# Optimization experiments

Measured on AMD Instinct MI355X. Metric: run time of the kernel, lower is better.

## Reference

```python
import jax, jax.numpy as jnp
import numpy as np

B, T, I = 256, 1024, 64
P, E, NOUT = 256, 128, 64
K = 2
TEMP = 8.0
LN_EPS = 1e-5


def setup_inputs() -> dict:
    key = jax.random.key(0)
    ks = jax.random.split(key, 10)
    lim_in = 1.0 / np.sqrt(I)
    lim_e = 1.0 / np.sqrt(E)
    return {
        "x": jax.random.normal(ks[0], (B, T, I), dtype=jnp.float32),
        "pointer_init": jax.random.uniform(ks[1], (B,), dtype=jnp.float32) * P,
        "W_in": jax.random.uniform(ks[2], (E, I), minval=-lim_in, maxval=lim_in),
        "b_in": jax.random.uniform(ks[3], (E,), minval=-lim_in, maxval=lim_in),
        "ln_w": jnp.ones((E,), jnp.float32),
        "ln_b": jnp.zeros((E,), jnp.float32),
        "jump_dest": jax.random.uniform(ks[4], (P,), dtype=jnp.float32) * P,
        "Wg": jax.random.uniform(ks[5], (1, E), minval=-lim_e, maxval=lim_e),
        "bg": jax.random.uniform(ks[6], (1,), minval=-lim_e, maxval=lim_e),
        "context_strength": jnp.float32(0.2),
        "Wo": jax.random.uniform(ks[7], (NOUT, E), minval=-lim_e, maxval=lim_e),
        "bo": jax.random.uniform(ks[8], (NOUT,), minval=-lim_e, maxval=lim_e),
    }


def _layer_norm(h, w, b):
    mu = jnp.mean(h, axis=-1, keepdims=True)
    var = jnp.mean((h - mu) ** 2, axis=-1, keepdims=True)
    return (h - mu) * jax.lax.rsqrt(var + LN_EPS) * w + b


def reference(x, pointer_init, W_in, b_in, ln_w, ln_b, jump_dest, Wg, bg, context_strength, Wo, bo):
    Bsz = x.shape[0]
    nP = jump_dest.shape[0]
    offsets = jnp.arange(-K, K + 1, dtype=jnp.int32)  # [5]
    batch_idx = jnp.arange(Bsz)[:, None]               # [B,1]
    ctx_scale = jax.nn.sigmoid(context_strength)
    half = nP / 2.0

    def step(carry, x_t):
        mem, hid, ptr = carry                          # [B,P,E], [B,E], [B]
        emb = jnp.tanh(x_t @ W_in.T + b_in)            # [B,E]
        base = jnp.clip(jnp.floor(ptr).astype(jnp.int32), 0, nP - 1)
        idx = jnp.mod(base[:, None] + offsets[None, :], nP)  # [B,5]
        delta = jnp.mod(idx.astype(x_t.dtype) - ptr[:, None] + half, nP) - half
        w = jax.nn.softmax(-(delta ** 2) / TEMP, axis=1)     # [B,5]
        nbh = jnp.take_along_axis(mem, idx[:, :, None], axis=1)  # [B,5,E]
        ctx = jnp.sum(w[:, :, None] * nbh, axis=1)               # [B,E]
        su = jnp.tanh(emb + ctx_scale * ctx + hid)               # [B,E]
        hid_new = _layer_norm(su, ln_w, ln_b)
        mem_new = mem.at[batch_idx, idx].add(w[:, :, None] * su[:, None, :])
        cur = jnp.clip(ptr.astype(jnp.int32), 0, nP - 1)
        jt = jump_dest[cur]                                      # [B]
        jl = (su @ Wg.T + bg)[:, 0]                              # [B]
        probs = jax.nn.sigmoid(jl)
        sj = (probs > 0.5).astype(x_t.dtype) - jax.lax.stop_gradient(probs) + probs
        walk = jnp.mod(ptr + 1.0, nP)
        ptr_new = jnp.where(sj > 0.5, jt, walk)
        return (mem_new, hid_new, ptr_new), None

    mem0 = jnp.zeros((Bsz, nP, W_in.shape[0]), x.dtype)
    hid0 = jnp.zeros((Bsz, W_in.shape[0]), x.dtype)
    (mem, hid, ptr), _ = jax.lax.scan(step, (mem0, hid0, pointer_init), jnp.swapaxes(x, 0, 1))
    logits = hid @ Wo.T + bo
    return logits
```

## Files before the change

### kernel.cpp

```cpp
#include <hip/hip_runtime.h>
#include <math.h>

#define Bn    256
#define Tn    1024
#define In    64
#define Pn    256
#define En    128
#define NOUTn 64
#define LN_EPS 1e-5f

#define C1f 0.3606737602222409f
#define K1f 0.8824969025845955f
#define K2f 0.6065306597126334f

typedef float f32x2 __attribute__((ext_vector_type(2)));

__device__ __forceinline__ float tanh_fast(float x) {
    float e = __builtin_amdgcn_exp2f(x * 2.88539008177793f);
    return 1.0f - 2.0f * __builtin_amdgcn_rcpf(e + 1.0f);
}
__device__ __forceinline__ f32x2 tanh2(f32x2 x) {
    f32x2 e;
    e[0] = __builtin_amdgcn_exp2f(x[0] * 2.88539008177793f);
    e[1] = __builtin_amdgcn_exp2f(x[1] * 2.88539008177793f);
    f32x2 r;
    r[0] = __builtin_amdgcn_rcpf(e[0] + 1.0f);
    r[1] = __builtin_amdgcn_rcpf(e[1] + 1.0f);
    return 1.0f - 2.0f * r;
}

template<int CTRL, int RMASK>
__device__ __forceinline__ float dpp_add(float x) {
    return x + __int_as_float(__builtin_amdgcn_update_dpp(
        0, __float_as_int(x), CTRL, RMASK, 0xF, false));
}
__device__ __forceinline__ void wave_sum64_x3(float& x, float& y, float& z) {
#define LVL(C, R) x = dpp_add<C, R>(x); y = dpp_add<C, R>(y); z = dpp_add<C, R>(z);
    LVL(0x111, 0xF)
    LVL(0x112, 0xF)
    LVL(0x114, 0xF)
    LVL(0x118, 0xF)
    LVL(0x142, 0xA)
    LVL(0x143, 0xC)
#undef LVL
    x = __int_as_float(__builtin_amdgcn_readlane(__float_as_int(x), 63));
    y = __int_as_float(__builtin_amdgcn_readlane(__float_as_int(y), 63));
    z = __int_as_float(__builtin_amdgcn_readlane(__float_as_int(z), 63));
}

#define STAGE_FLOATS (3 * 16 * En)
#define LDSF_FLOATS  (Pn * En + Pn + STAGE_FLOATS)
#define LDSF_BYTES   (LDSF_FLOATS * 4)

__global__ __launch_bounds__(192, 1)
void fused2_kernel(const float* __restrict__ x,
                   const float* __restrict__ pointer_init,
                   const float* __restrict__ W_in, const float* __restrict__ b_in,
                   const float* __restrict__ ln_w, const float* __restrict__ ln_b,
                   const float* __restrict__ jump_dest,
                   const float* __restrict__ Wg,  const float* __restrict__ bg,
                   const float* __restrict__ cs_ptr,
                   const float* __restrict__ Wo,  const float* __restrict__ bo,
                   float* __restrict__ out) {
    extern __shared__ float lds[];
    float* mem = lds;
    float* jd  = lds + Pn * En;
    float* stg = lds + Pn * En + Pn;

    const int b   = blockIdx.x;
    const int tid = threadIdx.x;

    if (tid >= 64) {
        const int p    = tid - 64;
        const int tq   = p >> 5;
        const int eidx = p & 31;
        float be[4];
        #pragma unroll
        for (int j = 0; j < 4; ++j) be[j] = b_in[eidx + 32 * j];
        const float* xb = x + (size_t)b * Tn * In;

#define PRODUCE(K, BUF) {                                                     \
    const int t0 = (K) * 16 + tq * 4;                                         \
    const float4* xr = (const float4*)(xb + t0 * In);      \
    float acc[4][4];                                                          \
    _Pragma("unroll")                                                         \
    for (int tt = 0; tt < 4; ++tt)                                            \
        _Pragma("unroll")                                                     \
        for (int j = 0; j < 4; ++j) acc[tt][j] = 0.f;                         \
    _Pragma("unroll")                                                         \
    for (int i4 = 0; i4 < 16; ++i4) {                                         \
        float4 xv[4];                                                         \
        _Pragma("unroll")                                                     \
        for (int tt = 0; tt < 4; ++tt) xv[tt] = xr[tt * 16 + i4];             \
        float4 wf[4];                                                         \
        _Pragma("unroll")                                                     \
        for (int j = 0; j < 4; ++j)                                           \
            wf[j] = *(const float4*)(W_in + (eidx + 32 * j) * In + i4 * 4);   \
        _Pragma("unroll")                                                     \
        for (int tt = 0; tt < 4; ++tt)                                        \
            _Pragma("unroll")                                                 \
            for (int j = 0; j < 4; ++j) {                                     \
                acc[tt][j] += xv[tt].x * wf[j].x;                             \
                acc[tt][j] += xv[tt].y * wf[j].y;                             \
                acc[tt][j] += xv[tt].z * wf[j].z;                             \
                acc[tt][j] += xv[tt].w * wf[j].w;                             \
            }                                                                 \
    }                                                                         \
    float* sg = stg + (BUF) * 2048 + tq * 512;                                \
    _Pragma("unroll")                                                         \
    for (int j = 0; j < 4; ++j) {                                             \
        float4 o;                                                             \
        o.x = tanh_fast(acc[0][j] + be[j]);                                   \
        o.y = tanh_fast(acc[1][j] + be[j]);                                   \
        o.z = tanh_fast(acc[2][j] + be[j]);                                   \
        o.w = tanh_fast(acc[3][j] + be[j]);                                   \
        *(float4*)(sg + (eidx + 32 * j) * 4) = o;                             \
    }                                                                         \
}
        PRODUCE(0, 0)
        PRODUCE(1, 1)
        __syncthreads();
        int buf = 2;
        for (int k = 0; k < 64; ++k) {
            if (k + 2 < 64) {
                PRODUCE(k + 2, buf)
                buf = (buf == 2) ? 0 : buf + 1;
            }
            __syncthreads();
        }
#undef PRODUCE
        __syncthreads();
        return;
    }

    const int l = tid;

    float4* m4 = (float4*)mem;
    for (int i = l; i < Pn * En / 4; i += 64) m4[i] = make_float4(0.f, 0.f, 0.f, 0.f);
    for (int i = l; i < Pn; i += 64) jd[i] = jump_dest[i];

    const f32x2 lnw = {ln_w[l], ln_w[l + 64]};
    const f32x2 lnb = {ln_b[l], ln_b[l + 64]};
    const f32x2 wg  = {Wg[l],   Wg[l + 64]};
    const float bgs = bg[0];
    const float cs  = 1.0f / (1.0f + expf(-cs_ptr[0]));
    f32x2 hid = {0.f, 0.f};

    float* myb = mem + 2 * l;

    float jl = 1.0f;
    float z0 = 0.f, z1 = 0.f, z2 = 1.f, z3 = 0.f, z4 = 0.f, inv = 1.f;
    float ptrW = 0.f; int baseW = 0; float jtW_pre = 0.f;
    f32x2 wnb0 = {0,0}, wnb1 = {0,0}, wnb2 = {0,0}, wnb3 = {0,0}, wnb4 = {0,0};
    float *wp0 = myb, *wp1 = myb, *wp2 = myb, *wp3 = myb, *wp4 = myb;
    float jptr  = pointer_init[b];
    int   jbase = (int)jptr; jbase = jbase > 255 ? 255 : jbase;
    float jz0, jz1, jz2 = 1.f, jz3, jz4, jinv;
    {
        const float frac = jptr - (float)jbase;
        const float r  = __builtin_amdgcn_exp2f(frac * C1f);
        const float ri = __builtin_amdgcn_exp2f(-frac * C1f);
        jz0 = K2f * ri * ri; jz1 = K1f * ri;
        jz3 = K1f * r;       jz4 = K2f * r * r;
        jinv = __builtin_amdgcn_rcpf(((jz0 + jz1) + (jz2 + jz3)) + jz4);
    }
    float *jp0 = mem + (((jbase + 254) & 255) << 7) + 2 * l;
    float *jp1 = mem + (((jbase + 255) & 255) << 7) + 2 * l;
    float *jp2 = mem + ((jbase) << 7) + 2 * l;
    float *jp3 = mem + (((jbase + 1) & 255) << 7) + 2 * l;
    float *jp4 = mem + (((jbase + 2) & 255) << 7) + 2 * l;
    f32x2 jnb0, jnb1, jnb2, jnb3, jnb4;
    float jjt;

    __syncthreads();

    jnb0 = *(f32x2*)jp0; jnb1 = *(f32x2*)jp1; jnb2 = *(f32x2*)jp2;
    jnb3 = *(f32x2*)jp3; jnb4 = *(f32x2*)jp4;
    jjt  = jd[jbase];

    const float* sa0 = stg + 4 * l;
    float4 A0 = *(const float4*)sa0;
    float4 A1 = *(const float4*)(sa0 + 256);

#define SSTEP(EC0, EC1) {                                                      \
    const bool JMP = jl > 0.0f;                         \
                  \
    const f32x2 ctxW = inv  * (((wnb0 * z0  + wnb1 * z1 )                      \
                              + (wnb2 * z2  + wnb3 * z3 )) + wnb4 * z4 );      \
    const f32x2 ctxJ = jinv * (((jnb0 * jz0 + jnb1 * jz1)                      \
                              + (jnb2 * jz2 + jnb3 * jz3)) + jnb4 * jz4);      \
    f32x2 ctx; ctx[0] = JMP ? ctxJ[0] : ctxW[0];                               \
               ctx[1] = JMP ? ctxJ[1] : ctxW[1];                               \
               \
    const float ptr  = JMP ? jptr  : ptrW;                                     \
    const int   base = JMP ? jbase : baseW;                                    \
    z0 = JMP ? jz0 : z0;  z1 = JMP ? jz1 : z1;                                 \
    z3 = JMP ? jz3 : z3;  z4 = JMP ? jz4 : z4;                                 \
    inv = JMP ? jinv : inv;                                                    \
    const f32x2 nb0 = JMP ? jnb0 : wnb0;                                       \
    const f32x2 nb1 = JMP ? jnb1 : wnb1;                                       \
    const f32x2 nb2 = JMP ? jnb2 : wnb2;                                       \
    const f32x2 nb3 = JMP ? jnb3 : wnb3;                                       \
    const f32x2 nb4 = JMP ? jnb4 : wnb4;                                       \
    float* p0 = JMP ? jp0 : wp0;  float* p1 = JMP ? jp1 : wp1;                 \
    float* p2 = JMP ? jp2 : wp2;  float* p3 = JMP ? jp3 : wp3;                 \
    float* p4 = JMP ? jp4 : wp4;                                               \
    const float jt_n = JMP ? jjt : jtW_pre;                                    \
                                      \
    f32x2 em; em[0] = (EC0); em[1] = (EC1);                                    \
    const f32x2 su = tanh2(em + cs * ctx + hid);                               \
    const f32x2 g  = su * inv;                                                 \
    const f32x2 m0v = nb0 + z0 * g, m1v = nb1 + z1 * g, m2v = nb2 + z2 * g,    \
                m3v = nb3 + z3 * g, m4v = nb4 + z4 * g;                        \
    *(f32x2*)p0 = m0v; *(f32x2*)p1 = m1v; *(f32x2*)p2 = m2v;                   \
    *(f32x2*)p3 = m3v; *(f32x2*)p4 = m4v;                                      \
      \
    baseW = (base + 1) & 255;                                                  \
    ptrW  = ptr + 1.0f; if (ptrW >= 256.0f) ptrW -= 256.0f;                    \
    wnb0 = m1v; wnb1 = m2v; wnb2 = m3v; wnb3 = m4v;                            \
    wp0 = p1; wp1 = p2; wp2 = p3; wp3 = p4;                                    \
    wp4 = mem + (((base + 3) & 255) << 7) + 2 * l;                             \
    wnb4 = *(f32x2*)wp4;                                                       \
    jtW_pre = jd[baseW];                                                       \
                 \
    jptr  = jt_n;                                                              \
    jbase = (int)jptr; jbase = jbase > 255 ? 255 : jbase;                      \
    {                                                                          \
        const float frac = jptr - (float)jbase;                                \
        const float r  = __builtin_amdgcn_exp2f(frac * C1f);                   \
        const float ri = __builtin_amdgcn_exp2f(-frac * C1f);                  \
        jz0 = K2f * ri * ri; jz1 = K1f * ri;                                   \
        jz3 = K1f * r;       jz4 = K2f * r * r;                                \
        jinv = __builtin_amdgcn_rcpf(((jz0 + jz1) + (jz2 + jz3)) + jz4);       \
    }                                                                          \
    jp0 = mem + (((jbase + 254) & 255) << 7) + 2 * l;                          \
    jp1 = mem + (((jbase + 255) & 255) << 7) + 2 * l;                          \
    jp2 = mem + ((jbase) << 7) + 2 * l;                                        \
    jp3 = mem + (((jbase + 1) & 255) << 7) + 2 * l;                            \
    jp4 = mem + (((jbase + 2) & 255) << 7) + 2 * l;                            \
    jnb0 = *(f32x2*)jp0; jnb1 = *(f32x2*)jp1; jnb2 = *(f32x2*)jp2;             \
    jnb3 = *(f32x2*)jp3; jnb4 = *(f32x2*)jp4;                                  \
    jjt  = jd[jbase];                                                          \
                                       \
    float s1 = su[0] + su[1];                                                  \
    const f32x2 sq = su * su;  float s2 = sq[0] + sq[1];                       \
    const f32x2 sg = su * wg;  float s3 = sg[0] + sg[1];                       \
    wave_sum64_x3(s1, s2, s3);                                                 \
    const float mu   = s1 * (1.0f / En);                                       \
    const float var  = s2 * (1.0f / En) - mu * mu;                             \
    const float rstd = __builtin_amdgcn_rsqf(var + LN_EPS);                    \
    hid = (su - mu) * rstd * lnw + lnb;                                        \
    jl  = s3 + bgs;                                                            \
}

    for (int k = 0; k < 64; ++k) {
        #pragma unroll 1
        for (int gi = 0; gi < 4; ++gi) {
            const int tb  = k * 4 + gi;
            int tbn = tb + 1; if (tbn > 255) tbn = 255;
            const float* sb = stg + ((tbn >> 2) % 3) * 2048 + (tbn & 3) * 512 + 4 * l;
            float4 B0 = *(const float4*)sb;
            float4 B1 = *(const float4*)(sb + 256);
            SSTEP(A0.x, A1.x)
            SSTEP(A0.y, A1.y)
            SSTEP(A0.z, A1.z)
            SSTEP(A0.w, A1.w)
            A0 = B0; A1 = B1;
        }
        __syncthreads();
    }
#undef SSTEP

    mem[l] = hid[0]; mem[64 + l] = hid[1];
    __syncthreads();
    const float4* w4 = (const float4*)(Wo + l * En);
    const float4* h4 = (const float4*)mem;
    float a0 = 0.f, a1 = 0.f, a2 = 0.f, a3 = 0.f;
    #pragma unroll
    for (int i = 0; i < En / 4; ++i) {
        float4 wv = w4[i]; float4 hv = h4[i];
        a0 += wv.x * hv.x; a1 += wv.y * hv.y; a2 += wv.z * hv.z; a3 += wv.w * hv.w;
    }
    out[b * NOUTn + l] = (a0 + a1) + (a2 + a3) + bo[l];
}

extern "C" void kernel_launch(void* const* d_in, const int* in_sizes, int n_in,
                              void* d_out, int out_size, void* d_ws, size_t ws_size,
                              hipStream_t stream) {
    const float* x            = (const float*)d_in[0];
    const float* pointer_init = (const float*)d_in[1];
    const float* W_in         = (const float*)d_in[2];
    const float* b_in         = (const float*)d_in[3];
    const float* ln_w         = (const float*)d_in[4];
    const float* ln_b         = (const float*)d_in[5];
    const float* jump_dest    = (const float*)d_in[6];
    const float* Wg           = (const float*)d_in[7];
    const float* bg           = (const float*)d_in[8];
    const float* cs           = (const float*)d_in[9];
    const float* Wo           = (const float*)d_in[10];
    const float* bo           = (const float*)d_in[11];
    float* out = (float*)d_out;
    (void)d_ws; (void)ws_size;

    (void)hipFuncSetAttribute((const void*)fused2_kernel,
                              hipFuncAttributeMaxDynamicSharedMemorySize, LDSF_BYTES);
    fused2_kernel<<<Bn, 192, LDSF_BYTES, stream>>>(
        x, pointer_init, W_in, b_in, ln_w, ln_b, jump_dest, Wg, bg, cs,
        Wo, bo, out);
}
```

Before: 483.0 us.

## Split embedding GEMM into separate kernel and stream scan inputs from global

Replaces the fused producer/consumer kernel, whose two extra wavefronts computed the input embedding into a triple-buffered LDS stage, with two kernels. A parallel emb_kernel writes the tanh embeddings to workspace, and a single-wave scan_kernel reads them from global memory with one-group-ahead prefetch. This drops the per-chunk __syncthreads and the producer work that shared the CU with the serial scan. In exchange it adds a global round trip of B*T*E floats through the workspace, and a global load latency on the scan's critical path.

```diff
diff --git a/kernel.cpp b/kernel.cpp
--- a/kernel.cpp
+++ b/kernel.cpp
@@ -48,92 +48,81 @@
     z = __int_as_float(__builtin_amdgcn_readlane(__float_as_int(z), 63));
 }
 
-#define STAGE_FLOATS (3 * 16 * En)
-#define LDSF_FLOATS  (Pn * En + Pn + STAGE_FLOATS)
-#define LDSF_BYTES   (LDSF_FLOATS * 4)
-
-__global__ __launch_bounds__(192, 1)
-void fused2_kernel(const float* __restrict__ x,
-                   const float* __restrict__ pointer_init,
-                   const float* __restrict__ W_in, const float* __restrict__ b_in,
-                   const float* __restrict__ ln_w, const float* __restrict__ ln_b,
-                   const float* __restrict__ jump_dest,
-                   const float* __restrict__ Wg,  const float* __restrict__ bg,
-                   const float* __restrict__ cs_ptr,
-                   const float* __restrict__ Wo,  const float* __restrict__ bo,
-                   float* __restrict__ out) {
+
+__global__ __launch_bounds__(256, 2)
+void emb_kernel(const float* __restrict__ x,
+                const float* __restrict__ W_in, const float* __restrict__ b_in,
+                float* __restrict__ emb) {
+    const int b    = blockIdx.x >> 4;
+    const int tc   = blockIdx.x & 15;
+    const int tid  = threadIdx.x;
+    const int tq   = tid >> 4;
+    const int eidx = tid & 15;
+
+    const int t0 = tc * 64 + tq * 4;
+    const float4* xr = (const float4*)(x + ((size_t)b * Tn + t0) * In);
+
+    float be[8];
+    #pragma unroll
+    for (int j = 0; j < 8; ++j) be[j] = b_in[eidx + 16 * j];
+
+    float acc[4][8];
+    #pragma unroll
+    for (int tt = 0; tt < 4; ++tt)
+        #pragma unroll
+        for (int j = 0; j < 8; ++j) acc[tt][j] = 0.f;
+
+    #pragma unroll
+    for (int i4 = 0; i4 < 16; ++i4) {
+        float4 xv[4];
+        #pragma unroll
+        for (int tt = 0; tt < 4; ++tt) xv[tt] = xr[tt * 16 + i4];
+        float4 wf[8];
+        #pragma unroll
+        for (int j = 0; j < 8; ++j)
+            wf[j] = *(const float4*)(W_in + (eidx + 16 * j) * In + i4 * 4);
+        #pragma unroll
+        for (int tt = 0; tt < 4; ++tt)
+            #pragma unroll
+            for (int j = 0; j < 8; ++j) {
+                acc[tt][j] += xv[tt].x * wf[j].x;
+                acc[tt][j] += xv[tt].y * wf[j].y;
+                acc[tt][j] += xv[tt].z * wf[j].z;
+                acc[tt][j] += xv[tt].w * wf[j].w;
+            }
+    }
+
+    const int g2 = tc * 16 + tq;
+    float* og = emb + ((size_t)b * 256 + g2) * 512;
+    #pragma unroll
+    for (int j = 0; j < 8; ++j) {
+        float4 o;
+        o.x = tanh_fast(acc[0][j] + be[j]);
+        o.y = tanh_fast(acc[1][j] + be[j]);
+        o.z = tanh_fast(acc[2][j] + be[j]);
+        o.w = tanh_fast(acc[3][j] + be[j]);
+        *(float4*)(og + (eidx + 16 * j) * 4) = o;
+    }
+}
+
+#define LDS2_FLOATS (Pn * En + Pn)
+#define LDS2_BYTES  (LDS2_FLOATS * 4)
+
+__global__ __launch_bounds__(64, 1)
+void scan_kernel(const float* __restrict__ emb,
+                 const float* __restrict__ pointer_init,
+                 const float* __restrict__ ln_w, const float* __restrict__ ln_b,
+                 const float* __restrict__ jump_dest,
+                 const float* __restrict__ Wg,  const float* __restrict__ bg,
+                 const float* __restrict__ cs_ptr,
+                 const float* __restrict__ Wo,  const float* __restrict__ bo,
+                 float* __restrict__ out) {
     extern __shared__ float lds[];
     float* mem = lds;
     float* jd  = lds + Pn * En;
-    float* stg = lds + Pn * En + Pn;
-
-    const int b   = blockIdx.x;
-    const int tid = threadIdx.x;
-
-    if (tid >= 64) {
-        const int p    = tid - 64;
-        const int tq   = p >> 5;
-        const int eidx = p & 31;
-        float be[4];
-        #pragma unroll
-        for (int j = 0; j < 4; ++j) be[j] = b_in[eidx + 32 * j];
-        const float* xb = x + (size_t)b * Tn * In;
-
-#define PRODUCE(K, BUF) {                                                     \
-    const int t0 = (K) * 16 + tq * 4;                                         \
-    const float4* xr = (const float4*)(xb + t0 * In);      \
-    float acc[4][4];                                                          \
-    _Pragma("unroll")                                                         \
-    for (int tt = 0; tt < 4; ++tt)                                            \
-        _Pragma("unroll")                                                     \
-        for (int j = 0; j < 4; ++j) acc[tt][j] = 0.f;                         \
-    _Pragma("unroll")                                                         \
-    for (int i4 = 0; i4 < 16; ++i4) {                                         \
-        float4 xv[4];                                                         \
-        _Pragma("unroll")                                                     \
-        for (int tt = 0; tt < 4; ++tt) xv[tt] = xr[tt * 16 + i4];             \
-        float4 wf[4];                                                         \
-        _Pragma("unroll")                                                     \
-        for (int j = 0; j < 4; ++j)                                           \
-            wf[j] = *(const float4*)(W_in + (eidx + 32 * j) * In + i4 * 4);   \
-        _Pragma("unroll")                                                     \
-        for (int tt = 0; tt < 4; ++tt)                                        \
-            _Pragma("unroll")                                                 \
-            for (int j = 0; j < 4; ++j) {                                     \
-                acc[tt][j] += xv[tt].x * wf[j].x;                             \
-                acc[tt][j] += xv[tt].y * wf[j].y;                             \
-                acc[tt][j] += xv[tt].z * wf[j].z;                             \
-                acc[tt][j] += xv[tt].w * wf[j].w;                             \
-            }                                                                 \
-    }                                                                         \
-    float* sg = stg + (BUF) * 2048 + tq * 512;                                \
-    _Pragma("unroll")                                                         \
-    for (int j = 0; j < 4; ++j) {                                             \
-        float4 o;                                                             \
-        o.x = tanh_fast(acc[0][j] + be[j]);                                   \
-        o.y = tanh_fast(acc[1][j] + be[j]);                                   \
-        o.z = tanh_fast(acc[2][j] + be[j]);                                   \
-        o.w = tanh_fast(acc[3][j] + be[j]);                                   \
-        *(float4*)(sg + (eidx + 32 * j) * 4) = o;                             \
-    }                                                                         \
-}
-        PRODUCE(0, 0)
-        PRODUCE(1, 1)
-        __syncthreads();
-        int buf = 2;
-        for (int k = 0; k < 64; ++k) {
-            if (k + 2 < 64) {
-                PRODUCE(k + 2, buf)
-                buf = (buf == 2) ? 0 : buf + 1;
-            }
-            __syncthreads();
-        }
-#undef PRODUCE
-        __syncthreads();
-        return;
-    }
-
-    const int l = tid;
+
+    const int b = blockIdx.x;
+    const int l = threadIdx.x;
 
     float4* m4 = (float4*)mem;
     for (int i = l; i < Pn * En / 4; i += 64) m4[i] = make_float4(0.f, 0.f, 0.f, 0.f);
@@ -178,20 +167,18 @@
     jnb3 = *(f32x2*)jp3; jnb4 = *(f32x2*)jp4;
     jjt  = jd[jbase];
 
-    const float* sa0 = stg + 4 * l;
-    float4 A0 = *(const float4*)sa0;
-    float4 A1 = *(const float4*)(sa0 + 256);
+    const float* eb = emb + (size_t)b * 256 * 512;
+    float4 A0 = *(const float4*)(eb + (size_t)l * 4);
+    float4 A1 = *(const float4*)(eb + 256 + (size_t)l * 4);
 
 #define SSTEP(EC0, EC1) {                                                      \
     const bool JMP = jl > 0.0f;                         \
-                  \
     const f32x2 ctxW = inv  * (((wnb0 * z0  + wnb1 * z1 )                      \
                               + (wnb2 * z2  + wnb3 * z3 )) + wnb4 * z4 );      \
     const f32x2 ctxJ = jinv * (((jnb0 * jz0 + jnb1 * jz1)                      \
                               + (jnb2 * jz2 + jnb3 * jz3)) + jnb4 * jz4);      \
     f32x2 ctx; ctx[0] = JMP ? ctxJ[0] : ctxW[0];                               \
                ctx[1] = JMP ? ctxJ[1] : ctxW[1];                               \
-               \
     const float ptr  = JMP ? jptr  : ptrW;                                     \
     const int   base = JMP ? jbase : baseW;                                    \
     z0 = JMP ? jz0 : z0;  z1 = JMP ? jz1 : z1;                                 \
@@ -206,7 +193,6 @@
     float* p2 = JMP ? jp2 : wp2;  float* p3 = JMP ? jp3 : wp3;                 \
     float* p4 = JMP ? jp4 : wp4;                                               \
     const float jt_n = JMP ? jjt : jtW_pre;                                    \
-                                      \
     f32x2 em; em[0] = (EC0); em[1] = (EC1);                                    \
     const f32x2 su = tanh2(em + cs * ctx + hid);                               \
     const f32x2 g  = su * inv;                                                 \
@@ -214,7 +200,6 @@
                 m3v = nb3 + z3 * g, m4v = nb4 + z4 * g;                        \
     *(f32x2*)p0 = m0v; *(f32x2*)p1 = m1v; *(f32x2*)p2 = m2v;                   \
     *(f32x2*)p3 = m3v; *(f32x2*)p4 = m4v;                                      \
-      \
     baseW = (base + 1) & 255;                                                  \
     ptrW  = ptr + 1.0f; if (ptrW >= 256.0f) ptrW -= 256.0f;                    \
     wnb0 = m1v; wnb1 = m2v; wnb2 = m3v; wnb3 = m4v;                            \
@@ -222,7 +207,6 @@
     wp4 = mem + (((base + 3) & 255) << 7) + 2 * l;                             \
     wnb4 = *(f32x2*)wp4;                                                       \
     jtW_pre = jd[baseW];                                                       \
-                 \
     jptr  = jt_n;                                                              \
     jbase = (int)jptr; jbase = jbase > 255 ? 255 : jbase;                      \
     {                                                                          \
@@ -241,7 +225,6 @@
     jnb0 = *(f32x2*)jp0; jnb1 = *(f32x2*)jp1; jnb2 = *(f32x2*)jp2;             \
     jnb3 = *(f32x2*)jp3; jnb4 = *(f32x2*)jp4;                                  \
     jjt  = jd[jbase];                                                          \
-                                       \
     float s1 = su[0] + su[1];                                                  \
     const f32x2 sq = su * su;  float s2 = sq[0] + sq[1];                       \
     const f32x2 sg = su * wg;  float s3 = sg[0] + sg[1];                       \
@@ -253,21 +236,17 @@
     jl  = s3 + bgs;                                                            \
 }
 
-    for (int k = 0; k < 64; ++k) {
-        #pragma unroll 1
-        for (int gi = 0; gi < 4; ++gi) {
-            const int tb  = k * 4 + gi;
-            int tbn = tb + 1; if (tbn > 255) tbn = 255;
-            const float* sb = stg + ((tbn >> 2) % 3) * 2048 + (tbn & 3) * 512 + 4 * l;
-            float4 B0 = *(const float4*)sb;
-            float4 B1 = *(const float4*)(sb + 256);
-            SSTEP(A0.x, A1.x)
-            SSTEP(A0.y, A1.y)
-            SSTEP(A0.z, A1.z)
-            SSTEP(A0.w, A1.w)
-            A0 = B0; A1 = B1;
-        }
-        __syncthreads();
+    #pragma unroll 1
+    for (int g2 = 0; g2 < 256; ++g2) {
+        int gn = g2 + 1; if (gn > 255) gn = 255;
+        const float* sb = eb + (size_t)gn * 512 + l * 4;
+        float4 B0 = *(const float4*)sb;
+        float4 B1 = *(const float4*)(sb + 256);
+        SSTEP(A0.x, A1.x)
+        SSTEP(A0.y, A1.y)
+        SSTEP(A0.z, A1.z)
+        SSTEP(A0.w, A1.w)
+        A0 = B0; A1 = B1;
     }
 #undef SSTEP
 
@@ -300,11 +279,12 @@
     const float* Wo           = (const float*)d_in[10];
     const float* bo           = (const float*)d_in[11];
     float* out = (float*)d_out;
-    (void)d_ws; (void)ws_size;
-
-    (void)hipFuncSetAttribute((const void*)fused2_kernel,
-                              hipFuncAttributeMaxDynamicSharedMemorySize, LDSF_BYTES);
-    fused2_kernel<<<Bn, 192, LDSF_BYTES, stream>>>(
-        x, pointer_init, W_in, b_in, ln_w, ln_b, jump_dest, Wg, bg, cs,
-        Wo, bo, out);
-}
+    float* emb = (float*)d_ws;
+
+    emb_kernel<<<Bn * 16, 256, 0, stream>>>(x, W_in, b_in, emb);
+
+    (void)hipFuncSetAttribute((const void*)scan_kernel,
+                              hipFuncAttributeMaxDynamicSharedMemorySize, LDS2_BYTES);
+    scan_kernel<<<Bn, 64, LDS2_BYTES, stream>>>(
+        emb, pointer_init, ln_w, ln_b, jump_dest, Wg, bg, cs, Wo, bo, out);
+}
```

After: 743.8 us. 54.0% more time.

## Precompute both context candidates ahead of jump decision and forward fresh writes

Applied to the files above, without the earlier changes.

Both the walk and jump context sums are now computed at the end of the previous step, so the per-step critical path after the jump decision is just a select plus tanh. Jump-neighbourhood loads are issued before the memory update. Any slot that overlaps rows written in the current step is then patched from the freshly computed values through a chain of selects. This shortens the serial dependency chain per timestep, at the cost of extra select logic and register pressure.

```diff
diff --git a/kernel.cpp b/kernel.cpp
--- a/kernel.cpp
+++ b/kernel.cpp
@@ -171,27 +171,30 @@
     float *jp4 = mem + (((jbase + 2) & 255) << 7) + 2 * l;
     f32x2 jnb0, jnb1, jnb2, jnb3, jnb4;
     float jjt;
+    f32x2 ctxW, ctxJ;
 
     __syncthreads();
 
     jnb0 = *(f32x2*)jp0; jnb1 = *(f32x2*)jp1; jnb2 = *(f32x2*)jp2;
     jnb3 = *(f32x2*)jp3; jnb4 = *(f32x2*)jp4;
     jjt  = jd[jbase];
+    ctxW = inv  * (((wnb0 * z0  + wnb1 * z1 ) + (wnb2 * z2  + wnb3 * z3 ))
+                   + wnb4 * z4 );
+    ctxJ = jinv * (((jnb0 * jz0 + jnb1 * jz1) + (jnb2 * jz2 + jnb3 * jz3))
+                   + jnb4 * jz4);
 
     const float* sa0 = stg + 4 * l;
     float4 A0 = *(const float4*)sa0;
     float4 A1 = *(const float4*)(sa0 + 256);
 
 #define SSTEP(EC0, EC1) {                                                      \
+     \
+    f32x2 em; em[0] = (EC0); em[1] = (EC1);                                    \
+    const f32x2 EW = em + cs * ctxW;                                           \
+    const f32x2 EJ = em + cs * ctxJ;                                           \
     const bool JMP = jl > 0.0f;                         \
-                  \
-    const f32x2 ctxW = inv  * (((wnb0 * z0  + wnb1 * z1 )                      \
-                              + (wnb2 * z2  + wnb3 * z3 )) + wnb4 * z4 );      \
-    const f32x2 ctxJ = jinv * (((jnb0 * jz0 + jnb1 * jz1)                      \
-                              + (jnb2 * jz2 + jnb3 * jz3)) + jnb4 * jz4);      \
-    f32x2 ctx; ctx[0] = JMP ? ctxJ[0] : ctxW[0];                               \
-               ctx[1] = JMP ? ctxJ[1] : ctxW[1];                               \
-               \
+    f32x2 E; E[0] = JMP ? EJ[0] : EW[0]; E[1] = JMP ? EJ[1] : EW[1];           \
+                                  \
     const float ptr  = JMP ? jptr  : ptrW;                                     \
     const int   base = JMP ? jbase : baseW;                                    \
     z0 = JMP ? jz0 : z0;  z1 = JMP ? jz1 : z1;                                 \
@@ -206,25 +209,22 @@
     float* p2 = JMP ? jp2 : wp2;  float* p3 = JMP ? jp3 : wp3;                 \
     float* p4 = JMP ? jp4 : wp4;                                               \
     const float jt_n = JMP ? jjt : jtW_pre;                                    \
-                                      \
-    f32x2 em; em[0] = (EC0); em[1] = (EC1);                                    \
-    const f32x2 su = tanh2(em + cs * ctx + hid);                               \
-    const f32x2 g  = su * inv;                                                 \
-    const f32x2 m0v = nb0 + z0 * g, m1v = nb1 + z1 * g, m2v = nb2 + z2 * g,    \
-                m3v = nb3 + z3 * g, m4v = nb4 + z4 * g;                        \
-    *(f32x2*)p0 = m0v; *(f32x2*)p1 = m1v; *(f32x2*)p2 = m2v;                   \
-    *(f32x2*)p3 = m3v; *(f32x2*)p4 = m4v;                                      \
-      \
-    baseW = (base + 1) & 255;                                                  \
-    ptrW  = ptr + 1.0f; if (ptrW >= 256.0f) ptrW -= 256.0f;                    \
-    wnb0 = m1v; wnb1 = m2v; wnb2 = m3v; wnb3 = m4v;                            \
-    wp0 = p1; wp1 = p2; wp2 = p3; wp3 = p4;                                    \
-    wp4 = mem + (((base + 3) & 255) << 7) + 2 * l;                             \
-    wnb4 = *(f32x2*)wp4;                                                       \
-    jtW_pre = jd[baseW];                                                       \
-                 \
+                      \
     jptr  = jt_n;                                                              \
     jbase = (int)jptr; jbase = jbase > 255 ? 255 : jbase;                      \
+    const int dov = (jbase - base) & 255;                                      \
+    jp0 = mem + (((jbase + 254) & 255) << 7) + 2 * l;                          \
+    jp1 = mem + (((jbase + 255) & 255) << 7) + 2 * l;                          \
+    jp2 = mem + ((jbase) << 7) + 2 * l;                                        \
+    jp3 = mem + (((jbase + 1) & 255) << 7) + 2 * l;                            \
+    jp4 = mem + (((jbase + 2) & 255) << 7) + 2 * l;                            \
+    const f32x2 jr0 = *(f32x2*)jp0, jr1 = *(f32x2*)jp1, jr2 = *(f32x2*)jp2,    \
+                jr3 = *(f32x2*)jp3, jr4 = *(f32x2*)jp4;                        \
+    float* wp4n = mem + (((base + 3) & 255) << 7) + 2 * l;                     \
+    const f32x2 wnb4n = *(f32x2*)wp4n;        \
+    const int   baseWn = (base + 1) & 255;                                     \
+    const float jtWn = jd[baseWn];                                             \
+    const float jjtn = jd[jbase];                                              \
     {                                                                          \
         const float frac = jptr - (float)jbase;                                \
         const float r  = __builtin_amdgcn_exp2f(frac * C1f);                   \
@@ -233,24 +233,43 @@
         jz3 = K1f * r;       jz4 = K2f * r * r;                                \
         jinv = __builtin_amdgcn_rcpf(((jz0 + jz1) + (jz2 + jz3)) + jz4);       \
     }                                                                          \
-    jp0 = mem + (((jbase + 254) & 255) << 7) + 2 * l;                          \
-    jp1 = mem + (((jbase + 255) & 255) << 7) + 2 * l;                          \
-    jp2 = mem + ((jbase) << 7) + 2 * l;                                        \
-    jp3 = mem + (((jbase + 1) & 255) << 7) + 2 * l;                            \
-    jp4 = mem + (((jbase + 2) & 255) << 7) + 2 * l;                            \
-    jnb0 = *(f32x2*)jp0; jnb1 = *(f32x2*)jp1; jnb2 = *(f32x2*)jp2;             \
-    jnb3 = *(f32x2*)jp3; jnb4 = *(f32x2*)jp4;                                  \
-    jjt  = jd[jbase];                                                          \
+                 \
+    const f32x2 su = tanh2(E + hid);                                           \
+    const f32x2 g  = su * inv;                                                 \
+    const f32x2 m0v = nb0 + z0 * g, m1v = nb1 + z1 * g, m2v = nb2 + z2 * g,    \
+                m3v = nb3 + z3 * g, m4v = nb4 + z4 * g;                        \
+    *(f32x2*)p0 = m0v; *(f32x2*)p1 = m1v; *(f32x2*)p2 = m2v;                   \
+    *(f32x2*)p3 = m3v; *(f32x2*)p4 = m4v;                                      \
+                                             \
+    baseW = baseWn;                                                            \
+    ptrW  = ptr + 1.0f; if (ptrW >= 256.0f) ptrW -= 256.0f;                    \
+    wnb0 = m1v; wnb1 = m2v; wnb2 = m3v; wnb3 = m4v; wnb4 = wnb4n;              \
+    wp0 = p1; wp1 = p2; wp2 = p3; wp3 = p4; wp4 = wp4n;                        \
+    jtW_pre = jtWn;                                                            \
+    jjt = jjtn;                                                                \
+                     \
+    const int si0 = dov, si1 = (1 + dov) & 255, si2 = (2 + dov) & 255,         \
+              si3 = (3 + dov) & 255, si4 = (4 + dov) & 255;                    \
+    jnb0 = si0==0?m0v: si0==1?m1v: si0==2?m2v: si0==3?m3v: si0==4?m4v: jr0;    \
+    jnb1 = si1==0?m0v: si1==1?m1v: si1==2?m2v: si1==3?m3v: si1==4?m4v: jr1;    \
+    jnb2 = si2==0?m0v: si2==1?m1v: si2==2?m2v: si2==3?m3v: si2==4?m4v: jr2;    \
+    jnb3 = si3==0?m0v: si3==1?m1v: si3==2?m2v: si3==3?m3v: si3==4?m4v: jr3;    \
+    jnb4 = si4==0?m0v: si4==1?m1v: si4==2?m2v: si4==3?m3v: si4==4?m4v: jr4;    \
+         \
+    ctxW = inv  * (((wnb0 * z0  + wnb1 * z1 ) + (wnb2 * z2  + wnb3 * z3 ))     \
+                   + wnb4 * z4 );                                              \
+    ctxJ = jinv * (((jnb0 * jz0 + jnb1 * jz1) + (jnb2 * jz2 + jnb3 * jz3))     \
+                   + jnb4 * jz4);                                              \
                                        \
     float s1 = su[0] + su[1];                                                  \
     const f32x2 sq = su * su;  float s2 = sq[0] + sq[1];                       \
-    const f32x2 sg = su * wg;  float s3 = sg[0] + sg[1];                       \
-    wave_sum64_x3(s1, s2, s3);                                                 \
+    const f32x2 sg = su * wg;  float s3v = sg[0] + sg[1];                      \
+    wave_sum64_x3(s1, s2, s3v);                                                \
     const float mu   = s1 * (1.0f / En);                                       \
     const float var  = s2 * (1.0f / En) - mu * mu;                             \
     const float rstd = __builtin_amdgcn_rsqf(var + LN_EPS);                    \
     hid = (su - mu) * rstd * lnw + lnb;                                        \
-    jl  = s3 + bgs;                                                            \
+    jl  = s3v + bgs;                                                           \
 }
 
     for (int k = 0; k < 64; ++k) {
```

Result: slower. 772.2 us (+59.9%).
